# Performance work log

Hardware: AMD Instinct MI355X
Metric: run time of the kernel (lower is better)

Reference implementation:

```python
import jax, jax.numpy as jnp
import numpy as np

D_MODEL = 1024
NUM_HEADS = 16
D_K = D_MODEL // NUM_HEADS


def setup_inputs() -> dict:
    key = jax.random.key(0)
    ks = jax.random.split(key, 9)
    s = 1.0 / np.sqrt(D_MODEL)
    x = jax.random.normal(ks[0], (4, 2048, D_MODEL), dtype=jnp.float32)
    Wq = jax.random.uniform(ks[1], (D_MODEL, D_MODEL), jnp.float32, -s, s)
    bq = jax.random.uniform(ks[2], (D_MODEL,), jnp.float32, -s, s)
    Wk = jax.random.uniform(ks[3], (D_MODEL, D_MODEL), jnp.float32, -s, s)
    bk = jax.random.uniform(ks[4], (D_MODEL,), jnp.float32, -s, s)
    Wv = jax.random.uniform(ks[5], (D_MODEL, D_MODEL), jnp.float32, -s, s)
    bv = jax.random.uniform(ks[6], (D_MODEL,), jnp.float32, -s, s)
    Wo = jax.random.uniform(ks[7], (D_MODEL, D_MODEL), jnp.float32, -s, s)
    bo = jax.random.uniform(ks[8], (D_MODEL,), jnp.float32, -s, s)
    return {"x": x, "Wq": Wq, "bq": bq, "Wk": Wk, "bk": bk,
            "Wv": Wv, "bv": bv, "Wo": Wo, "bo": bo}


def reference(x, Wq, bq, Wk, bk, Wv, bv, Wo, bo):
    B, T, C = x.shape
    H, Dk = NUM_HEADS, D_K
    # linear projections (torch Linear: x @ W.T + b; here W stored as [in,out])
    q = (x @ Wq + bq).reshape(B, T, H, Dk).transpose(0, 2, 1, 3)  # [B,H,T,Dk]
    k = (x @ Wk + bk).reshape(B, T, H, Dk).transpose(0, 2, 1, 3)
    v = (x @ Wv + bv).reshape(B, T, H, Dk).transpose(0, 2, 1, 3)
    scores = jnp.einsum("bhtd,bhsd->bhts", q, k) / jnp.sqrt(jnp.float32(Dk))
    attn = jax.nn.softmax(scores, axis=-1)  # [B,H,T,T]
    context = jnp.einsum("bhts,bhsd->bhtd", attn, v)
    context = context.transpose(0, 2, 1, 3).reshape(B, T, C)
    return context @ Wo + bo
```

## Files before the change

kernel.cpp:

```cpp
#include <hip/hip_runtime.h>
#include <hip/hip_bf16.h>
#include <stdint.h>

typedef short bf16x8 __attribute__((ext_vector_type(8)));
typedef float f32x4  __attribute__((ext_vector_type(4)));

#define MFMA16(a, b, c) __builtin_amdgcn_mfma_f32_16x16x32_bf16((a), (b), (c), 0, 0, 0)

__device__ __forceinline__ unsigned short f2bf(float f) {
    union { float f; unsigned int u; } v; v.f = f;
    unsigned int u = v.u;
    u += 0x7fffu + ((u >> 16) & 1u);
    return (unsigned short)(u >> 16);
}

__device__ __forceinline__ unsigned int trunc_pk(float a, float b) {
    return (__float_as_uint(a) >> 16) | (__float_as_uint(b) & 0xffff0000u);
}

__device__ __forceinline__ float exp2f_fast(float x) {
#if __has_builtin(__builtin_amdgcn_exp2f)
    return __builtin_amdgcn_exp2f(x);
#else
    return exp2f(x);
#endif
}

__device__ __forceinline__ void g2lds16(const void* g, void* l) {
    __builtin_amdgcn_global_load_lds(
        (const __attribute__((address_space(1))) void*)g,
        (__attribute__((address_space(3))) void*)l, 16, 0, 0);
}


__global__ __launch_bounds__(256) void convert_x_kernel(
    const float4* __restrict__ src, ushort4* __restrict__ dst)
{
    int i = blockIdx.x * 256 + threadIdx.x;
    float4 v = src[i];
    ushort4 o;
    o.x = f2bf(v.x); o.y = f2bf(v.y); o.z = f2bf(v.z); o.w = f2bf(v.w);
    dst[i] = o;
}

__global__ __launch_bounds__(256) void transpose_w_kernel(
    const float* __restrict__ src, unsigned short* __restrict__ dst)
{
    __shared__ float tile[64][65];
    const int k0 = blockIdx.x * 64, n0 = blockIdx.y * 64;
    const int tx = threadIdx.x & 63, ty = threadIdx.x >> 6;
    #pragma unroll
    for (int i = 0; i < 64; i += 4)
        tile[ty + i][tx] = src[(size_t)(k0 + ty + i) * 1024 + n0 + tx];
    __syncthreads();
    #pragma unroll
    for (int i = 0; i < 64; i += 4)
        dst[(size_t)(n0 + ty + i) * 1024 + k0 + tx] = f2bf(tile[tx][ty + i]);
}


#define QSCALE 0.18033688011112042f

template <int MODE>
__global__ __launch_bounds__(256, 2) void gemm_bt(
    const unsigned short* __restrict__ A, const unsigned short* __restrict__ Bt,
    const float* __restrict__ b0, const float* __restrict__ b1, const float* __restrict__ b2,
    unsigned short* __restrict__ Qb, unsigned short* __restrict__ Kb,
    unsigned short* __restrict__ Vt, float* __restrict__ out)
{
    __shared__ alignas(16) unsigned short As[128 * 32];
    __shared__ alignas(16) unsigned short Bs[128 * 32];

    const int t = threadIdx.x;
    const int m0 = blockIdx.y * 128, n0 = blockIdx.x * 128;
    const int lane = t & 63, w = t >> 6, quad = lane >> 4, c16 = lane & 15;
    const int moff = (w >> 1) * 64, noff = (w & 1) * 64;

    f32x4 acc[4][4];
    #pragma unroll
    for (int i = 0; i < 4; ++i)
        #pragma unroll
        for (int j = 0; j < 4; ++j)
            acc[i][j] = (f32x4){0.f, 0.f, 0.f, 0.f};

    const unsigned short* Ag = A + (size_t)(m0 + (t >> 2)) * 1024 + (t & 3) * 8;
    const unsigned short* Bg = Bt + (size_t)(n0 + (t >> 2)) * 1024 + (t & 3) * 8;
    unsigned short* Asl = As + t * 8;
    unsigned short* Bsl = Bs + t * 8;

    for (int k0 = 0; k0 < 1024; k0 += 32) {
        g2lds16(Ag + k0,             Asl);
        g2lds16(Ag + 64 * 1024 + k0, Asl + 2048);
        g2lds16(Bg + k0,             Bsl);
        g2lds16(Bg + 64 * 1024 + k0, Bsl + 2048);
        __syncthreads();

        bf16x8 af[4], bfr[4];
        #pragma unroll
        for (int ms = 0; ms < 4; ++ms)
            af[ms] = *(const bf16x8*)(As + (moff + ms * 16 + c16) * 32 + quad * 8);
        #pragma unroll
        for (int ns = 0; ns < 4; ++ns)
            bfr[ns] = *(const bf16x8*)(Bs + (noff + ns * 16 + c16) * 32 + quad * 8);
        #pragma unroll
        for (int ms = 0; ms < 4; ++ms)
            #pragma unroll
            for (int ns = 0; ns < 4; ++ns)
                acc[ms][ns] = MFMA16(af[ms], bfr[ns], acc[ms][ns]);
        __syncthreads();
    }

    #pragma unroll
    for (int ns = 0; ns < 4; ++ns) {
        const int n = n0 + noff + ns * 16 + c16;
        if (MODE == 0) {
            const int mat = n >> 10, nn = n & 1023;
            const int h = nn >> 6, d = nn & 63;
            const float bias = (mat == 0) ? b0[nn] : ((mat == 1) ? b1[nn] : b2[nn]);
            #pragma unroll
            for (int ms = 0; ms < 4; ++ms) {
                const int mbase = m0 + moff + ms * 16 + quad * 4;
                const int b = mbase >> 11, tbase = mbase & 2047;
                const int bh = b * 16 + h;
                if (mat == 2) {
                    ushort4 pk;
                    pk.x = f2bf(acc[ms][ns][0] + bias);
                    pk.y = f2bf(acc[ms][ns][1] + bias);
                    pk.z = f2bf(acc[ms][ns][2] + bias);
                    pk.w = f2bf(acc[ms][ns][3] + bias);
                    *(ushort4*)(Vt + ((size_t)bh * 64 + d) * 2048 + tbase) = pk;
                } else {
                    #pragma unroll
                    for (int r = 0; r < 4; ++r) {
                        float v = acc[ms][ns][r] + bias;
                        if (mat == 0) v *= QSCALE;
                        unsigned short* dst = (mat == 0) ? Qb : Kb;
                        dst[((size_t)bh * 2048 + tbase + r) * 64 + d] = f2bf(v);
                    }
                }
            }
        } else {
            const float bias = b0[n];
            #pragma unroll
            for (int ms = 0; ms < 4; ++ms) {
                #pragma unroll
                for (int r = 0; r < 4; ++r) {
                    const int m = m0 + moff + ms * 16 + quad * 4 + r;
                    out[(size_t)m * 1024 + n] = acc[ms][ns][r] + bias;
                }
            }
        }
    }
}


__global__ __launch_bounds__(128, 2) void attn_kernel(
    const unsigned short* __restrict__ Qb, const unsigned short* __restrict__ Kb,
    const unsigned short* __restrict__ Vt, unsigned short* __restrict__ ctx)
{
    __shared__ alignas(16) unsigned short Ks[64 * 64];
    __shared__ alignas(16) unsigned short Vs[64 * 64];

    const int t = threadIdx.x, w = t >> 6, lane = t & 63;
    const int quad = lane >> 4, c16 = lane & 15;
    const int bh = blockIdx.y;
    const int qbase = blockIdx.x * 128 + w * 64;

    bf16x8 qf[4][2];
    #pragma unroll
    for (int mt = 0; mt < 4; ++mt) {
        const unsigned short* Qp = Qb + ((size_t)bh * 2048 + qbase + mt * 16 + c16) * 64;
        qf[mt][0] = *(const bf16x8*)(Qp + quad * 8);
        qf[mt][1] = *(const bf16x8*)(Qp + 32 + quad * 8);
    }

    float l_r[4] = {0.f, 0.f, 0.f, 0.f};
    f32x4 O[4][4];
    #pragma unroll
    for (int mt = 0; mt < 4; ++mt)
        #pragma unroll
        for (int dc = 0; dc < 4; ++dc) O[mt][dc] = (f32x4){0.f, 0.f, 0.f, 0.f};

    const int sgrp = (t & 7) ^ ((t >> 3) & 7);
    const unsigned short* Kgl = Kb + (size_t)bh * 131072 + (size_t)(t >> 3) * 64 + sgrp * 8;
    const unsigned short* Vgl = Vt + (size_t)bh * 131072 + (size_t)(t >> 3) * 2048 + sgrp * 8;
    unsigned short* Ksl = Ks + t * 8;
    unsigned short* Vsl = Vs + t * 8;
    const f32x4 fzero = {0.f, 0.f, 0.f, 0.f};

    for (int s0 = 0; s0 < 2048; s0 += 64) {
        #pragma unroll
        for (int q = 0; q < 4; ++q) {
            g2lds16(Kgl + s0 * 64 + q * 1024,  Ksl + q * 1024);
            g2lds16(Vgl + s0 + q * 32768,      Vsl + q * 1024);
        }
        __syncthreads();

        #pragma unroll
        for (int ct = 0; ct < 4; ++ct) {
            const int key = ct * 16 + c16;
            const bf16x8 kf0 = *(const bf16x8*)(Ks + key * 64 + ((quad ^ (key & 7)) << 3));
            const bf16x8 kf1 = *(const bf16x8*)(Ks + key * 64 + (((4 + quad) ^ (key & 7)) << 3));

            uint2 vf[4];
            const int g = ct * 2 + (quad >> 1);
            #pragma unroll
            for (int dc = 0; dc < 4; ++dc) {
                const int d = dc * 16 + c16;
                vf[dc] = *(const uint2*)(Vs + d * 64 + ((g ^ (d & 7)) << 3) + (quad & 1) * 4);
            }

            #pragma unroll
            for (int mt = 0; mt < 4; ++mt) {
                f32x4 sa = MFMA16(kf0, qf[mt][0], fzero);
                sa = MFMA16(kf1, qf[mt][1], sa);
                const float p0 = exp2f_fast(sa[0]);
                const float p1 = exp2f_fast(sa[1]);
                const float p2 = exp2f_fast(sa[2]);
                const float p3 = exp2f_fast(sa[3]);
                l_r[mt] += (p0 + p1) + (p2 + p3);
                union { bf16x8 v; unsigned int d[4]; } af;
                af.d[0] = trunc_pk(p0, p1);
                af.d[1] = trunc_pk(p2, p3);
                af.d[2] = 0u; af.d[3] = 0u;
                #pragma unroll
                for (int dc = 0; dc < 4; ++dc) {
                    union { bf16x8 v; uint2 u[2]; } bfv;
                    bfv.u[0] = vf[dc]; bfv.u[1] = vf[dc];
                    O[mt][dc] = MFMA16(af.v, bfv.v, O[mt][dc]);
                }
            }
        }
        __syncthreads();
    }

    #pragma unroll
    for (int mt = 0; mt < 4; ++mt) {
        l_r[mt] += __shfl_xor(l_r[mt], 16);
        l_r[mt] += __shfl_xor(l_r[mt], 32);
    }

    const int b = bh >> 4, h = bh & 15;
    #pragma unroll
    for (int mt = 0; mt < 4; ++mt) {
        float inv[4];
        #pragma unroll
        for (int r = 0; r < 4; ++r)
            inv[r] = 1.0f / __shfl(l_r[mt], quad * 4 + r);
        #pragma unroll
        for (int dc = 0; dc < 4; ++dc)
            #pragma unroll
            for (int r = 0; r < 4; ++r) {
                const int row = qbase + mt * 16 + quad * 4 + r;
                ctx[((size_t)(b * 2048 + row)) * 1024 + h * 64 + dc * 16 + c16] =
                    f2bf(O[mt][dc][r] * inv[r]);
            }
    }
}


extern "C" void kernel_launch(void* const* d_in, const int* in_sizes, int n_in,
                              void* d_out, int out_size, void* d_ws, size_t ws_size,
                              hipStream_t stream)
{
    const float* x  = (const float*)d_in[0];
    const float* Wq = (const float*)d_in[1];
    const float* bq = (const float*)d_in[2];
    const float* Wk = (const float*)d_in[3];
    const float* bk = (const float*)d_in[4];
    const float* Wv = (const float*)d_in[5];
    const float* bv = (const float*)d_in[6];
    const float* Wo = (const float*)d_in[7];
    const float* bo = (const float*)d_in[8];
    float* out = (float*)d_out;

    char* ws = (char*)d_ws;
    unsigned short* xb    = (unsigned short*)(ws);
    unsigned short* Wqkvt = (unsigned short*)(ws + (16u << 20));
    unsigned short* Wot   = (unsigned short*)(ws + (22u << 20));
    unsigned short* Vt    = (unsigned short*)(ws + (24u << 20));
    unsigned short* Qb    = (unsigned short*)((char*)d_out);
    unsigned short* Kb    = (unsigned short*)((char*)d_out + (16u << 20));

    convert_x_kernel<<<8192, 256, 0, stream>>>((const float4*)x, (ushort4*)xb);
    dim3 tg(16, 16);
    transpose_w_kernel<<<tg, 256, 0, stream>>>(Wq, Wqkvt);
    transpose_w_kernel<<<tg, 256, 0, stream>>>(Wk, Wqkvt + (1u << 20));
    transpose_w_kernel<<<tg, 256, 0, stream>>>(Wv, Wqkvt + (2u << 20));
    transpose_w_kernel<<<tg, 256, 0, stream>>>(Wo, Wot);

    gemm_bt<0><<<dim3(24, 64), 256, 0, stream>>>(xb, Wqkvt, bq, bk, bv, Qb, Kb, Vt, nullptr);
    attn_kernel<<<dim3(16, 64), 128, 0, stream>>>(Qb, Kb, Vt, xb );
    gemm_bt<1><<<dim3(8, 64), 256, 0, stream>>>(xb, Wot, bo, nullptr, nullptr,
                                                nullptr, nullptr, nullptr, out);
}
```

Before: 303.0 us.

## Use K16 MFMA for PV, remap attention blocks, merge weight transposes

The P·V product moves from the 16x16x32 MFMA padded with zeros to a native 16x16x16 bf16 MFMA when that builtin exists, which removes the wasted half of each PV instruction. Attention blocks are remapped so consecutive workgroups spread across heads, which is meant to change cache locality and load balance. The four weight-transpose launches are merged into one 3D-grid launch, with Wo stored right after Wqkv. The K16 path depends on the compiler exposing that builtin on gfx950, and the changed block order could hurt L2 reuse of K and V.

```diff
diff --git a/kernel.cpp b/kernel.cpp
--- a/kernel.cpp
+++ b/kernel.cpp
@@ -3,9 +3,20 @@
 #include <stdint.h>
 
 typedef short bf16x8 __attribute__((ext_vector_type(8)));
+typedef short bf16x4 __attribute__((ext_vector_type(4)));
 typedef float f32x4  __attribute__((ext_vector_type(4)));
 
 #define MFMA16(a, b, c) __builtin_amdgcn_mfma_f32_16x16x32_bf16((a), (b), (c), 0, 0, 0)
+
+#if __has_builtin(__builtin_amdgcn_mfma_f32_16x16x16bf16_1k)
+  #define HAVE_K16 1
+  #define MFMAK16(a, b, c) __builtin_amdgcn_mfma_f32_16x16x16bf16_1k((a), (b), (c), 0, 0, 0)
+#elif __has_builtin(__builtin_amdgcn_mfma_f32_16x16x16_bf16)
+  #define HAVE_K16 1
+  #define MFMAK16(a, b, c) __builtin_amdgcn_mfma_f32_16x16x16_bf16((a), (b), (c), 0, 0, 0)
+#else
+  #define HAVE_K16 0
+#endif
 
 __device__ __forceinline__ unsigned short f2bf(float f) {
     union { float f; unsigned int u; } v; v.f = f;
@@ -43,10 +54,15 @@
     dst[i] = o;
 }
 
-__global__ __launch_bounds__(256) void transpose_w_kernel(
-    const float* __restrict__ src, unsigned short* __restrict__ dst)
+__global__ __launch_bounds__(256) void transpose_w4_kernel(
+    const float* __restrict__ W0, const float* __restrict__ W1,
+    const float* __restrict__ W2, const float* __restrict__ W3,
+    unsigned short* __restrict__ dst_base)
 {
     __shared__ float tile[64][65];
+    const int z = blockIdx.z;
+    const float* src = (z == 0) ? W0 : (z == 1) ? W1 : (z == 2) ? W2 : W3;
+    unsigned short* dst = dst_base + ((size_t)z << 20);
     const int k0 = blockIdx.x * 64, n0 = blockIdx.y * 64;
     const int tx = threadIdx.x & 63, ty = threadIdx.x >> 6;
     #pragma unroll
@@ -163,8 +179,10 @@
 
     const int t = threadIdx.x, w = t >> 6, lane = t & 63;
     const int quad = lane >> 4, c16 = lane & 15;
-    const int bh = blockIdx.y;
-    const int qbase = blockIdx.x * 128 + w * 64;
+    const int L = blockIdx.y * 16 + blockIdx.x;
+    const int bh = ((L & 7) << 3) + (L >> 7);
+    const int qt = (L >> 3) & 15;
+    const int qbase = qt * 128 + w * 64;
 
     bf16x8 qf[4][2];
     #pragma unroll
@@ -219,6 +237,17 @@
                 const float p2 = exp2f_fast(sa[2]);
                 const float p3 = exp2f_fast(sa[3]);
                 l_r[mt] += (p0 + p1) + (p2 + p3);
+#if HAVE_K16
+                union { bf16x4 v; unsigned int d[2]; } af;
+                af.d[0] = trunc_pk(p0, p1);
+                af.d[1] = trunc_pk(p2, p3);
+                #pragma unroll
+                for (int dc = 0; dc < 4; ++dc) {
+                    union { bf16x4 v; uint2 u; } bv;
+                    bv.u = vf[dc];
+                    O[mt][dc] = MFMAK16(af.v, bv.v, O[mt][dc]);
+                }
+#else
                 union { bf16x8 v; unsigned int d[4]; } af;
                 af.d[0] = trunc_pk(p0, p1);
                 af.d[1] = trunc_pk(p2, p3);
@@ -229,6 +258,7 @@
                     bfv.u[0] = vf[dc]; bfv.u[1] = vf[dc];
                     O[mt][dc] = MFMA16(af.v, bfv.v, O[mt][dc]);
                 }
+#endif
             }
         }
         __syncthreads();
@@ -277,17 +307,13 @@
     char* ws = (char*)d_ws;
     unsigned short* xb    = (unsigned short*)(ws);
     unsigned short* Wqkvt = (unsigned short*)(ws + (16u << 20));
-    unsigned short* Wot   = (unsigned short*)(ws + (22u << 20));
     unsigned short* Vt    = (unsigned short*)(ws + (24u << 20));
+    unsigned short* Wot   = Wqkvt + (3u << 20);
     unsigned short* Qb    = (unsigned short*)((char*)d_out);
     unsigned short* Kb    = (unsigned short*)((char*)d_out + (16u << 20));
 
     convert_x_kernel<<<8192, 256, 0, stream>>>((const float4*)x, (ushort4*)xb);
-    dim3 tg(16, 16);
-    transpose_w_kernel<<<tg, 256, 0, stream>>>(Wq, Wqkvt);
-    transpose_w_kernel<<<tg, 256, 0, stream>>>(Wk, Wqkvt + (1u << 20));
-    transpose_w_kernel<<<tg, 256, 0, stream>>>(Wv, Wqkvt + (2u << 20));
-    transpose_w_kernel<<<tg, 256, 0, stream>>>(Wo, Wot);
+    transpose_w4_kernel<<<dim3(16, 16, 4), 256, 0, stream>>>(Wq, Wk, Wv, Wo, Wqkvt);
 
     gemm_bt<0><<<dim3(24, 64), 256, 0, stream>>>(xb, Wqkvt, bq, bk, bv, Qb, Kb, Vt, nullptr);
     attn_kernel<<<dim3(16, 64), 128, 0, stream>>>(Qb, Kb, Vt, xb );
```

New measurement: 284.3 us. -6.2%, faster.
